# Optimization experiments

Hardware: AMD Instinct MI355X
Metric: run time of the kernel (lower is better)

Reference implementation:

```python
import jax, jax.numpy as jnp
import numpy as np

NUM_HEADS = 8
HEAD_DIM = 64


def setup_inputs() -> dict:
    key = jax.random.key(0)
    k0, k1, k2, k3 = jax.random.split(key, 4)
    B, S, Dm = 16, 4096, 512
    x = jax.random.normal(k0, (B, S, Dm), dtype=jnp.float32)
    W_q = jax.random.normal(k1, (Dm, NUM_HEADS * HEAD_DIM), dtype=jnp.float32) * 0.02
    W_k = jax.random.normal(k2, (Dm, NUM_HEADS * HEAD_DIM), dtype=jnp.float32) * 0.02
    W_v = jax.random.normal(k3, (Dm, NUM_HEADS * HEAD_DIM), dtype=jnp.float32) * 0.02
    return {"x": x, "W_q": W_q, "W_k": W_k, "W_v": W_v}


def reference(x, W_q, W_k, W_v):
    B, S, _ = x.shape
    H, D = NUM_HEADS, HEAD_DIM
    # projections -> (B, S, H, D); NOTE: original keeps layout (B,S,H,D)
    # without transposing, so tf.matmul batches over (B,S): attention is
    # computed ACROSS HEADS per token (HxH scores), unscaled. Faithful here.
    q = (x @ W_q).reshape(B, S, H, D)
    k = (x @ W_k).reshape(B, S, H, D)
    v = (x @ W_v).reshape(B, S, H, D)
    scores = jnp.einsum("bshd,bstd->bsht", q, k)  # (B,S,H,H)
    attn = jax.nn.softmax(scores, axis=-1)
    out = jnp.einsum("bsht,bstd->bshd", attn, v)  # (B,S,H,D)
    return out.reshape(B, S, H * D)
```

## Files before the change

### kernel.cpp

```cpp
#include <hip/hip_runtime.h>
#include <hip/hip_bf16.h>

typedef __bf16 bf16_t;
typedef __bf16 bf16x8 __attribute__((ext_vector_type(8)));
typedef float  f32x4  __attribute__((ext_vector_type(4)));

#define DM    512
#define NQKV  1536
#define NTOK  65536
#define TM    32
#define QSTR  1544

__device__ __align__(16) bf16_t g_wt2[(size_t)NQKV * DM];

#define MEMFENCE asm volatile("" ::: "memory")

__global__ void prep_w2(const float* __restrict__ Wq,
                        const float* __restrict__ Wk,
                        const float* __restrict__ Wv) {
    int flat = blockIdx.x * 256 + threadIdx.x;
    int l  = flat & 63;
    int kg = l >> 4, lr = l & 15;
    int t2 = flat >> 6;
    int ni = t2 % 12;
    int t3 = t2 / 12;
    int s  = t3 & 15, w = t3 >> 4;
    int n  = w * 192 + ni * 16 + lr;
    int k0 = s * 32 + kg * 8;
    int mat = n >> 9, nn = n & 511;
    const float* W = (mat == 0) ? Wq : ((mat == 1) ? Wk : Wv);
    bf16x8 v;
#pragma unroll
    for (int e = 0; e < 8; ++e) v[e] = (bf16_t)W[(k0 + e) * DM + nn];
    *(bf16x8*)(g_wt2 + (size_t)flat * 8) = v;
}

__global__ __launch_bounds__(512, 1) void fused_mha(
    const float* __restrict__ x, float* __restrict__ out) {
    extern __shared__ char sm[];

    const int tid = threadIdx.x;
    const int l   = tid & 63, w = tid >> 6;
    const int lr  = l & 15,  kg = l >> 4;
    const size_t tok0 = (size_t)blockIdx.x * TM;

    {
        const int r = tid >> 4, tj = tid & 15, r7 = r & 7;
        const float* xp = x + (tok0 + r) * DM;
#pragma unroll
        for (int j = 0; j < 4; ++j) {
            int c = tj + j * 16;
            float4 f0 = *(const float4*)(xp + c * 8);
            float4 f1 = *(const float4*)(xp + c * 8 + 4);
            bf16x8 v;
            v[0] = (bf16_t)f0.x; v[1] = (bf16_t)f0.y;
            v[2] = (bf16_t)f0.z; v[3] = (bf16_t)f0.w;
            v[4] = (bf16_t)f1.x; v[5] = (bf16_t)f1.y;
            v[6] = (bf16_t)f1.z; v[7] = (bf16_t)f1.w;
            *(bf16x8*)(sm + r * 1024 + ((c ^ r7) << 4)) = v;
        }
    }

    const bf16_t* gw = g_wt2 + ((size_t)w * 16 * 12 * 64 + l) * 8;
    bf16x8 bufA[12], bufB[12];
#pragma unroll
    for (int ni = 0; ni < 12; ++ni)
        bufA[ni] = *(const bf16x8*)(gw + ni * 512);
#pragma unroll
    for (int ni = 0; ni < 12; ++ni)
        bufB[ni] = *(const bf16x8*)(gw + 6144 + ni * 512);

    asm volatile("s_waitcnt lgkmcnt(0)" ::: "memory");
    __builtin_amdgcn_s_barrier();
    MEMFENCE;

    f32x4 acc[2][12];
#pragma unroll
    for (int a = 0; a < 2; ++a)
#pragma unroll
        for (int b = 0; b < 12; ++b) acc[a][b] = (f32x4){0.f, 0.f, 0.f, 0.f};

    const int sx = (lr & 7) << 4;

#define AREAD(dst, s_) do {                                                   \
        dst[0] = *(const bf16x8*)(sm + lr * 1024 +                            \
                                  (((s_) * 64 + kg * 16) ^ sx));              \
        dst[1] = *(const bf16x8*)(sm + 16384 + lr * 1024 +                    \
                                  (((s_) * 64 + kg * 16) ^ sx));              \
    } while (0)

#define MFMA_STEP(AF, BUF)                                                    \
    _Pragma("unroll")                                                         \
    for (int mi = 0; mi < 2; ++mi)                                            \
    _Pragma("unroll")                                                         \
    for (int ni = 0; ni < 12; ++ni)                                           \
        acc[mi][ni] = __builtin_amdgcn_mfma_f32_16x16x32_bf16(                \
            AF[mi], BUF[ni], acc[mi][ni], 0, 0, 0);

#pragma unroll
    for (int sp = 0; sp < 8; ++sp) {
        const int s0 = sp * 2, s1 = s0 + 1;
        bf16x8 af0[2], af1[2];
        AREAD(af0, s0);
        AREAD(af1, s1);
        MFMA_STEP(af0, bufA);
        if (sp < 7) {
#pragma unroll
            for (int ni = 0; ni < 12; ++ni)
                bufA[ni] = *(const bf16x8*)(gw + (s0 + 2) * 6144 + ni * 512);
        }
        MFMA_STEP(af1, bufB);
        if (sp < 7) {
#pragma unroll
            for (int ni = 0; ni < 12; ++ni)
                bufB[ni] = *(const bf16x8*)(gw + (s1 + 2) * 6144 + ni * 512);
        }
    }
#undef AREAD
#undef MFMA_STEP

    MEMFENCE;
    __builtin_amdgcn_s_barrier();
    MEMFENCE;

    bf16_t* qkv = (bf16_t*)sm;
#pragma unroll
    for (int mi = 0; mi < 2; ++mi)
#pragma unroll
        for (int ni = 0; ni < 12; ++ni) {
            int col = w * 192 + ni * 16 + lr;
#pragma unroll
            for (int i = 0; i < 4; ++i) {
                int token = mi * 16 + kg * 4 + i;
                qkv[token * QSTR + col] = (bf16_t)acc[mi][ni][i];
            }
        }
    asm volatile("s_waitcnt lgkmcnt(0)" ::: "memory");
    __builtin_amdgcn_s_barrier();
    MEMFENCE;

    const int tok = tid >> 4, tj = tid & 15, h = tj & 7, d0 = (tj >> 3) << 5;
    const bf16_t* base = qkv + tok * QSTR;

    float qv[32];
    {
        const bf16_t* qp = base + h * 64 + d0;
#pragma unroll
        for (int j = 0; j < 4; ++j) {
            bf16x8 q8 = *(const bf16x8*)(qp + 8 * j);
#pragma unroll
            for (int e = 0; e < 8; ++e) qv[8 * j + e] = (float)q8[e];
        }
    }

    float s[8];
#pragma unroll
    for (int t = 0; t < 8; ++t) {
        const bf16_t* kp = base + 512 + t * 64 + d0;
        float a = 0.f;
#pragma unroll
        for (int j = 0; j < 4; ++j) {
            bf16x8 k8 = *(const bf16x8*)(kp + 8 * j);
#pragma unroll
            for (int e = 0; e < 8; ++e) a += qv[8 * j + e] * (float)k8[e];
        }
        s[t] = a;
    }
#pragma unroll
    for (int t = 0; t < 8; ++t) s[t] += __shfl_xor(s[t], 8, 64);

    float m = s[0];
#pragma unroll
    for (int t = 1; t < 8; ++t) m = fmaxf(m, s[t]);
    float p[8], psum = 0.f;
#pragma unroll
    for (int t = 0; t < 8; ++t) {
        p[t] = exp2f((s[t] - m) * 1.44269504088896f);
        psum += p[t];
    }
    float inv = 1.0f / psum;

    float o[32];
#pragma unroll
    for (int e = 0; e < 32; ++e) o[e] = 0.f;
#pragma unroll
    for (int t = 0; t < 8; ++t) {
        float pt = p[t] * inv;
        const bf16_t* vp = base + 1024 + t * 64 + d0;
#pragma unroll
        for (int j = 0; j < 4; ++j) {
            bf16x8 v8 = *(const bf16x8*)(vp + 8 * j);
#pragma unroll
            for (int e = 0; e < 8; ++e) o[8 * j + e] += pt * (float)v8[e];
        }
    }

    float* op = out + (tok0 + tok) * DM + h * 64 + d0;
#pragma unroll
    for (int j = 0; j < 8; ++j) {
        float4 o4 = {o[4 * j], o[4 * j + 1], o[4 * j + 2], o[4 * j + 3]};
        *(float4*)(op + 4 * j) = o4;
    }
}

extern "C" void kernel_launch(void* const* d_in, const int* in_sizes, int n_in,
                              void* d_out, int out_size, void* d_ws, size_t ws_size,
                              hipStream_t stream) {
    (void)d_ws; (void)ws_size; (void)n_in; (void)out_size;
    const float* x  = (const float*)d_in[0];
    const float* Wq = (const float*)d_in[1];
    const float* Wk = (const float*)d_in[2];
    const float* Wv = (const float*)d_in[3];
    float* out = (float*)d_out;

    int ntok = in_sizes[0] / DM;
    prep_w2<<<384, 256, 0, stream>>>(Wq, Wk, Wv);
    size_t lds = (size_t)TM * QSTR * sizeof(bf16_t);
    fused_mha<<<ntok / TM, 512, lds, stream>>>(x, out);
}
```

Baseline: 202.8 us.

## Raise token tile to 48 rows and shrink weight prefetch buffer depth

Grows the per-block token tile from 32 to 48, so each weight fragment loaded from global memory feeds three MFMA row tiles instead of two. This cuts weight traffic per token. To make room in registers for the larger accumulator (3x12 tiles), the weight double buffer is cut to a one-step-ahead prefetch split into two 6-wide halves. The grid now has a ragged last block with bounds checks, and the attention phase loops twice per thread. Risks include higher register pressure, a shallower prefetch that exposes more global load latency, uneven work in the second attention pass, and a larger LDS footprint.

```diff
diff --git a/kernel.cpp b/kernel.cpp
--- a/kernel.cpp
+++ b/kernel.cpp
@@ -8,7 +8,7 @@
 #define DM    512
 #define NQKV  1536
 #define NTOK  65536
-#define TM    32
+#define TM    48
 #define QSTR  1544
 
 __device__ __align__(16) bf16_t g_wt2[(size_t)NQKV * DM];
@@ -43,89 +43,90 @@
     const int l   = tid & 63, w = tid >> 6;
     const int lr  = l & 15,  kg = l >> 4;
     const size_t tok0 = (size_t)blockIdx.x * TM;
+    const int ntb = (int)(((size_t)NTOK - tok0) < TM ? (NTOK - tok0) : TM);
 
     {
-        const int r = tid >> 4, tj = tid & 15, r7 = r & 7;
-        const float* xp = x + (tok0 + r) * DM;
-#pragma unroll
-        for (int j = 0; j < 4; ++j) {
-            int c = tj + j * 16;
-            float4 f0 = *(const float4*)(xp + c * 8);
-            float4 f1 = *(const float4*)(xp + c * 8 + 4);
-            bf16x8 v;
-            v[0] = (bf16_t)f0.x; v[1] = (bf16_t)f0.y;
-            v[2] = (bf16_t)f0.z; v[3] = (bf16_t)f0.w;
-            v[4] = (bf16_t)f1.x; v[5] = (bf16_t)f1.y;
-            v[6] = (bf16_t)f1.z; v[7] = (bf16_t)f1.w;
-            *(bf16x8*)(sm + r * 1024 + ((c ^ r7) << 4)) = v;
+        const int rbase = tid >> 5;
+        const int cj    = tid & 31;
+#pragma unroll
+        for (int p = 0; p < 3; ++p) {
+            int r = p * 16 + rbase;
+            if (r < ntb) {
+                const float* xp = x + (tok0 + r) * DM;
+                int r7 = r & 7;
+#pragma unroll
+                for (int jj = 0; jj < 2; ++jj) {
+                    int c = cj + jj * 32;
+                    float4 f0 = *(const float4*)(xp + c * 8);
+                    float4 f1 = *(const float4*)(xp + c * 8 + 4);
+                    bf16x8 v;
+                    v[0] = (bf16_t)f0.x; v[1] = (bf16_t)f0.y;
+                    v[2] = (bf16_t)f0.z; v[3] = (bf16_t)f0.w;
+                    v[4] = (bf16_t)f1.x; v[5] = (bf16_t)f1.y;
+                    v[6] = (bf16_t)f1.z; v[7] = (bf16_t)f1.w;
+                    *(bf16x8*)(sm + r * 1024 + ((c ^ r7) << 4)) = v;
+                }
+            }
         }
     }
 
     const bf16_t* gw = g_wt2 + ((size_t)w * 16 * 12 * 64 + l) * 8;
-    bf16x8 bufA[12], bufB[12];
-#pragma unroll
-    for (int ni = 0; ni < 12; ++ni)
-        bufA[ni] = *(const bf16x8*)(gw + ni * 512);
-#pragma unroll
-    for (int ni = 0; ni < 12; ++ni)
-        bufB[ni] = *(const bf16x8*)(gw + 6144 + ni * 512);
+    bf16x8 bx[6], by[6];
+#pragma unroll
+    for (int ni = 0; ni < 6; ++ni) bx[ni] = *(const bf16x8*)(gw + ni * 512);
+#pragma unroll
+    for (int ni = 0; ni < 6; ++ni) by[ni] = *(const bf16x8*)(gw + (6 + ni) * 512);
 
     asm volatile("s_waitcnt lgkmcnt(0)" ::: "memory");
     __builtin_amdgcn_s_barrier();
     MEMFENCE;
 
-    f32x4 acc[2][12];
-#pragma unroll
-    for (int a = 0; a < 2; ++a)
+    f32x4 acc[3][12];
+#pragma unroll
+    for (int a = 0; a < 3; ++a)
 #pragma unroll
         for (int b = 0; b < 12; ++b) acc[a][b] = (f32x4){0.f, 0.f, 0.f, 0.f};
 
     const int sx = (lr & 7) << 4;
 
-#define AREAD(dst, s_) do {                                                   \
-        dst[0] = *(const bf16x8*)(sm + lr * 1024 +                            \
-                                  (((s_) * 64 + kg * 16) ^ sx));              \
-        dst[1] = *(const bf16x8*)(sm + 16384 + lr * 1024 +                    \
-                                  (((s_) * 64 + kg * 16) ^ sx));              \
-    } while (0)
-
-#define MFMA_STEP(AF, BUF)                                                    \
-    _Pragma("unroll")                                                         \
-    for (int mi = 0; mi < 2; ++mi)                                            \
-    _Pragma("unroll")                                                         \
-    for (int ni = 0; ni < 12; ++ni)                                           \
-        acc[mi][ni] = __builtin_amdgcn_mfma_f32_16x16x32_bf16(                \
-            AF[mi], BUF[ni], acc[mi][ni], 0, 0, 0);
-
-#pragma unroll
-    for (int sp = 0; sp < 8; ++sp) {
-        const int s0 = sp * 2, s1 = s0 + 1;
-        bf16x8 af0[2], af1[2];
-        AREAD(af0, s0);
-        AREAD(af1, s1);
-        MFMA_STEP(af0, bufA);
-        if (sp < 7) {
-#pragma unroll
-            for (int ni = 0; ni < 12; ++ni)
-                bufA[ni] = *(const bf16x8*)(gw + (s0 + 2) * 6144 + ni * 512);
-        }
-        MFMA_STEP(af1, bufB);
-        if (sp < 7) {
-#pragma unroll
-            for (int ni = 0; ni < 12; ++ni)
-                bufB[ni] = *(const bf16x8*)(gw + (s1 + 2) * 6144 + ni * 512);
+#pragma unroll
+    for (int s = 0; s < 16; ++s) {
+        bf16x8 af[3];
+#pragma unroll
+        for (int mi = 0; mi < 3; ++mi)
+            af[mi] = *(const bf16x8*)(sm + (mi * 16 + lr) * 1024 +
+                                      ((s * 64 + kg * 16) ^ sx));
+#pragma unroll
+        for (int mi = 0; mi < 3; ++mi)
+#pragma unroll
+            for (int ni = 0; ni < 6; ++ni)
+                acc[mi][ni] = __builtin_amdgcn_mfma_f32_16x16x32_bf16(
+                    af[mi], bx[ni], acc[mi][ni], 0, 0, 0);
+        if (s < 15) {
+#pragma unroll
+            for (int ni = 0; ni < 6; ++ni)
+                bx[ni] = *(const bf16x8*)(gw + ((s + 1) * 12 + ni) * 512);
+        }
+#pragma unroll
+        for (int mi = 0; mi < 3; ++mi)
+#pragma unroll
+            for (int ni = 0; ni < 6; ++ni)
+                acc[mi][6 + ni] = __builtin_amdgcn_mfma_f32_16x16x32_bf16(
+                    af[mi], by[ni], acc[mi][6 + ni], 0, 0, 0);
+        if (s < 15) {
+#pragma unroll
+            for (int ni = 0; ni < 6; ++ni)
+                by[ni] = *(const bf16x8*)(gw + ((s + 1) * 12 + 6 + ni) * 512);
         }
     }
-#undef AREAD
-#undef MFMA_STEP
-
-    MEMFENCE;
+
+    asm volatile("s_waitcnt lgkmcnt(0)" ::: "memory");
     __builtin_amdgcn_s_barrier();
     MEMFENCE;
 
     bf16_t* qkv = (bf16_t*)sm;
 #pragma unroll
-    for (int mi = 0; mi < 2; ++mi)
+    for (int mi = 0; mi < 3; ++mi)
 #pragma unroll
         for (int ni = 0; ni < 12; ++ni) {
             int col = w * 192 + ni * 16 + lr;
@@ -139,67 +140,73 @@
     __builtin_amdgcn_s_barrier();
     MEMFENCE;
 
-    const int tok = tid >> 4, tj = tid & 15, h = tj & 7, d0 = (tj >> 3) << 5;
-    const bf16_t* base = qkv + tok * QSTR;
-
-    float qv[32];
-    {
-        const bf16_t* qp = base + h * 64 + d0;
-#pragma unroll
-        for (int j = 0; j < 4; ++j) {
-            bf16x8 q8 = *(const bf16x8*)(qp + 8 * j);
-#pragma unroll
-            for (int e = 0; e < 8; ++e) qv[8 * j + e] = (float)q8[e];
-        }
-    }
-
-    float s[8];
-#pragma unroll
-    for (int t = 0; t < 8; ++t) {
-        const bf16_t* kp = base + 512 + t * 64 + d0;
-        float a = 0.f;
-#pragma unroll
-        for (int j = 0; j < 4; ++j) {
-            bf16x8 k8 = *(const bf16x8*)(kp + 8 * j);
-#pragma unroll
-            for (int e = 0; e < 8; ++e) a += qv[8 * j + e] * (float)k8[e];
-        }
-        s[t] = a;
-    }
-#pragma unroll
-    for (int t = 0; t < 8; ++t) s[t] += __shfl_xor(s[t], 8, 64);
-
-    float m = s[0];
-#pragma unroll
-    for (int t = 1; t < 8; ++t) m = fmaxf(m, s[t]);
-    float p[8], psum = 0.f;
-#pragma unroll
-    for (int t = 0; t < 8; ++t) {
-        p[t] = exp2f((s[t] - m) * 1.44269504088896f);
-        psum += p[t];
-    }
-    float inv = 1.0f / psum;
-
-    float o[32];
-#pragma unroll
-    for (int e = 0; e < 32; ++e) o[e] = 0.f;
-#pragma unroll
-    for (int t = 0; t < 8; ++t) {
-        float pt = p[t] * inv;
-        const bf16_t* vp = base + 1024 + t * 64 + d0;
-#pragma unroll
-        for (int j = 0; j < 4; ++j) {
-            bf16x8 v8 = *(const bf16x8*)(vp + 8 * j);
-#pragma unroll
-            for (int e = 0; e < 8; ++e) o[8 * j + e] += pt * (float)v8[e];
-        }
-    }
-
-    float* op = out + (tok0 + tok) * DM + h * 64 + d0;
-#pragma unroll
-    for (int j = 0; j < 8; ++j) {
-        float4 o4 = {o[4 * j], o[4 * j + 1], o[4 * j + 2], o[4 * j + 3]};
-        *(float4*)(op + 4 * j) = o4;
+#pragma unroll
+    for (int p = 0; p < 2; ++p) {
+        const int tok = p * 32 + (tid >> 4);
+        if (tok < ntb) {
+            const int tj = tid & 15, h = tj & 7, d0 = (tj >> 3) << 5;
+            const bf16_t* base = qkv + tok * QSTR;
+
+            float qv[32];
+            {
+                const bf16_t* qp = base + h * 64 + d0;
+#pragma unroll
+                for (int j = 0; j < 4; ++j) {
+                    bf16x8 q8 = *(const bf16x8*)(qp + 8 * j);
+#pragma unroll
+                    for (int e = 0; e < 8; ++e) qv[8 * j + e] = (float)q8[e];
+                }
+            }
+
+            float s[8];
+#pragma unroll
+            for (int t = 0; t < 8; ++t) {
+                const bf16_t* kp = base + 512 + t * 64 + d0;
+                float a = 0.f;
+#pragma unroll
+                for (int j = 0; j < 4; ++j) {
+                    bf16x8 k8 = *(const bf16x8*)(kp + 8 * j);
+#pragma unroll
+                    for (int e = 0; e < 8; ++e) a += qv[8 * j + e] * (float)k8[e];
+                }
+                s[t] = a;
+            }
+#pragma unroll
+            for (int t = 0; t < 8; ++t) s[t] += __shfl_xor(s[t], 8, 64);
+
+            float m = s[0];
+#pragma unroll
+            for (int t = 1; t < 8; ++t) m = fmaxf(m, s[t]);
+            float pr[8], psum = 0.f;
+#pragma unroll
+            for (int t = 0; t < 8; ++t) {
+                pr[t] = exp2f((s[t] - m) * 1.44269504088896f);
+                psum += pr[t];
+            }
+            float inv = 1.0f / psum;
+
+            float o[32];
+#pragma unroll
+            for (int e = 0; e < 32; ++e) o[e] = 0.f;
+#pragma unroll
+            for (int t = 0; t < 8; ++t) {
+                float pt = pr[t] * inv;
+                const bf16_t* vp = base + 1024 + t * 64 + d0;
+#pragma unroll
+                for (int j = 0; j < 4; ++j) {
+                    bf16x8 v8 = *(const bf16x8*)(vp + 8 * j);
+#pragma unroll
+                    for (int e = 0; e < 8; ++e) o[8 * j + e] += pt * (float)v8[e];
+                }
+            }
+
+            float* op = out + (tok0 + tok) * DM + h * 64 + d0;
+#pragma unroll
+            for (int j = 0; j < 8; ++j) {
+                float4 o4 = {o[4 * j], o[4 * j + 1], o[4 * j + 2], o[4 * j + 3]};
+                *(float4*)(op + 4 * j) = o4;
+            }
+        }
     }
 }
 
@@ -214,7 +221,8 @@
     float* out = (float*)d_out;
 
     int ntok = in_sizes[0] / DM;
+    int grid = (ntok + TM - 1) / TM;
     prep_w2<<<384, 256, 0, stream>>>(Wq, Wk, Wv);
     size_t lds = (size_t)TM * QSTR * sizeof(bf16_t);
-    fused_mha<<<ntok / TM, 512, lds, stream>>>(x, out);
+    fused_mha<<<grid, 512, lds, stream>>>(x, out);
 }
```

Result: slower. 223.5 us (+10.2%).
